# Performance work log

Measured on AMD Instinct MI355X. Metric: run time of the kernel, lower is better.

## Reference

```python
import jax, jax.numpy as jnp
import numpy as np


def setup_inputs() -> dict:
    key = jax.random.key(0)
    k = jax.random.split(key, 5)
    bs, n_heads, ch, n_obj, emb = 4, 8, 64, 8, 64
    ih = iw = 32
    T = ih * iw
    return {
        "qkv": jax.random.normal(k[0], (bs, 3 * n_heads * ch, T), dtype=jnp.float32),
        "bboxes": jax.random.uniform(k[1], (bs, n_obj, 5), dtype=jnp.float32),
        "null_prompt_emb": jax.random.normal(k[2], (bs, emb, T), dtype=jnp.float32),
        "prompt_emb": jax.random.normal(k[3], (bs, emb, T), dtype=jnp.float32),
        "W_prompt": jax.random.normal(k[4], (3 * n_heads * ch, emb), dtype=jnp.float32) * 0.02,
        "n_heads": n_heads,
        "image_h": ih,
        "image_w": iw,
    }


def _region_masks(bboxes, h, w):
    # Faithful translation of get_region: bbox unpacked as (x, y, width, height, obj_idx).
    # Returns float masks [b, n_obj, h*w].
    x, y, bw, bh = bboxes[..., 0], bboxes[..., 1], bboxes[..., 2], bboxes[..., 3]
    i0 = jnp.minimum(float(h) - 1.0, jnp.floor(y * h))
    j0 = jnp.minimum(float(w) - 1.0, jnp.floor(x * w))
    i1 = i0 + jnp.maximum(1.0, jnp.ceil(bh * h))
    j1 = j0 + jnp.maximum(1.0, jnp.ceil(bw * w))
    ii = jnp.arange(h, dtype=jnp.float32)
    jj = jnp.arange(w, dtype=jnp.float32)
    mi = (ii >= i0[..., None]) & (ii < i1[..., None])          # [b, n, h]
    mj = (jj >= j0[..., None]) & (jj < j1[..., None])          # [b, n, w]
    m = (mi[..., :, None] & mj[..., None, :]).astype(jnp.float32)  # [b, n, h, w]
    return m.reshape(m.shape[0], m.shape[1], h * w)


def reference(qkv, bboxes, null_prompt_emb, prompt_emb, W_prompt, n_heads, image_h, image_w):
    bs, width, T = qkv.shape
    ch = width // (3 * n_heads)
    scale = float(ch) ** -0.25  # 1/sqrt(sqrt(ch))

    def split3(x):
        x = x.reshape(bs * n_heads, 3 * ch, T)
        return x[:, :ch], x[:, ch:2 * ch], x[:, 2 * ch:]

    q, k, v = split3(qkv)
    # to_prompt_token is a 1x1 Conv1d (no bias) == matmul over the channel dim
    nq, nk, nv = split3(jnp.einsum('oc,bct->bot', W_prompt, null_prompt_emb))
    pq, pk, pv = split3(jnp.einsum('oc,bct->bot', W_prompt, prompt_emb))

    def attn(qh, kh, vh, col_mask=None):
        w = jnp.einsum('bct,bcs->bts', qh * scale, kh * scale)
        if col_mask is not None:
            w = jnp.where(col_mask[:, None, :] > 0.5, w, -1e9)
        w = jax.nn.softmax(w.astype(jnp.float32), axis=-1).astype(qh.dtype)
        return jnp.einsum('bts,bcs->btc', w, vh)  # [bs*heads, T, ch]

    # global (null-prompt) attention
    a_null = attn(q + nq, k + nk, v + nv)

    # per-object masked attention, blended by region masks
    masks = _region_masks(bboxes, image_h, image_w)       # [bs, n_obj, T]
    masks = jnp.repeat(masks, n_heads, axis=0)            # [(bs*heads), n_obj, T]
    qf, kf, vf = q + pq, k + pk, v + pv
    a_fg = jnp.zeros_like(a_null)
    counter = jnp.zeros((bs * n_heads, T, 1), dtype=jnp.float32)
    for o in range(masks.shape[1]):  # small fixed loop over objects
        m = masks[:, o]                                   # [bs*heads, T]
        a_fg = a_fg + m[:, :, None] * attn(qf, kf, vf, col_mask=m)
        counter = counter + m[:, :, None]
    fg = counter > 0.5
    a_final = jnp.where(fg, a_fg, a_null) / jnp.where(fg, counter, 1.0)
    return jnp.transpose(a_final, (0, 2, 1)).reshape(bs, n_heads * ch, T)
```

## Files before the change

### kernel.cpp

```cpp
#include <hip/hip_runtime.h>
#include <math.h>

#define BS 4
#define NH 8
#define TT 1024
#define WROWS 1536
#define NOBJ 8
#define NT 65536

#define QNT_OFF  0
#define KNT_OFF  2097152
#define VNCS_OFF 4194304
#define QFT_OFF  6291456
#define KFT_OFF  8388608
#define VFT_OFF  10485760

typedef __attribute__((ext_vector_type(8))) short short8;
typedef __attribute__((ext_vector_type(4))) float v4f;

__device__ __forceinline__ short f2bf(float f) {
    unsigned u = __float_as_uint(f);
    u = (u + 0x7FFF + ((u >> 16) & 1)) >> 16;
    return (short)u;
}
__device__ __forceinline__ unsigned p2(float a, float b) {
    return (unsigned)(unsigned short)f2bf(a) | ((unsigned)(unsigned short)f2bf(b) << 16);
}

__device__ __forceinline__ void get_region(const float* __restrict__ bb,
                                           int& i0, int& j0, int& hh, int& ww) {
    float x = bb[0], y = bb[1], bw = bb[2], bh = bb[3];
    float i0f = fminf(31.0f, floorf(y * 32.0f));
    float j0f = fminf(31.0f, floorf(x * 32.0f));
    float i1f = i0f + fmaxf(1.0f, ceilf(bh * 32.0f));
    float j1f = j0f + fmaxf(1.0f, ceilf(bw * 32.0f));
    i0 = (int)i0f; j0 = (int)j0f;
    int i1 = min(32, (int)i1f);
    int j1 = min(32, (int)j1f);
    hh = i1 - i0; ww = j1 - j0;
}

__global__ __launch_bounds__(256)
void fuse_kernel(const float* __restrict__ qkv, const float* __restrict__ nEmb,
                 const float* __restrict__ pEmb, const float* __restrict__ W,
                 short* __restrict__ wsS) {
    __shared__ float WtT[64][68];
    __shared__ float En[64][64];
    __shared__ float Ep[64][64];
    short* sbuf = (short*)&WtT[0][0];
    int t0 = blockIdx.x * 64;
    int r0 = blockIdx.y * 64;
    int b  = blockIdx.z;
    int tid = threadIdx.x;
    int half = tid >> 4;
    int q4 = (tid & 15) * 4;
#pragma unroll
    for (int p = 0; p < 4; ++p) {
        int rr = p * 16 + half;
        float4 w4 = *(const float4*)&W[(r0 + rr) * 64 + q4];
        WtT[q4 + 0][rr] = w4.x; WtT[q4 + 1][rr] = w4.y;
        WtT[q4 + 2][rr] = w4.z; WtT[q4 + 3][rr] = w4.w;
        int e = p * 16 + half;
        *(float4*)&En[e][q4] = *(const float4*)&nEmb[(b * 64 + e) * TT + t0 + q4];
        *(float4*)&Ep[e][q4] = *(const float4*)&pEmb[(b * 64 + e) * TT + t0 + q4];
    }
    __syncthreads();
    int tr = tid >> 4, tc = tid & 15;
    float an[4][4] = {{0.f}}, ap[4][4] = {{0.f}};
#pragma unroll 8
    for (int e = 0; e < 64; ++e) {
        float4 w4 = *(const float4*)&WtT[e][tr * 4];
        float4 n4 = *(const float4*)&En[e][tc * 4];
        float4 p4 = *(const float4*)&Ep[e][tc * 4];
        float w[4]  = {w4.x, w4.y, w4.z, w4.w};
        float nn[4] = {n4.x, n4.y, n4.z, n4.w};
        float pp[4] = {p4.x, p4.y, p4.z, p4.w};
#pragma unroll
        for (int i = 0; i < 4; ++i)
#pragma unroll
            for (int j = 0; j < 4; ++j) {
                an[i][j] += w[i] * nn[j];
                ap[i][j] += w[i] * pp[j];
            }
    }
    int sec = (r0 % 192) / 64;
    int h = r0 / 192, bh = b * 8 + h;
    float sc = (sec == 0) ? 0.125f : 1.0f;
#pragma unroll
    for (int i = 0; i < 4; ++i) {
        int r = r0 + tr * 4 + i;
        float4 x4 = *(const float4*)&qkv[(b * WROWS + r) * TT + t0 + tc * 4];
        an[i][0] = (an[i][0] + x4.x) * sc; an[i][1] = (an[i][1] + x4.y) * sc;
        an[i][2] = (an[i][2] + x4.z) * sc; an[i][3] = (an[i][3] + x4.w) * sc;
        ap[i][0] = (ap[i][0] + x4.x) * sc; ap[i][1] = (ap[i][1] + x4.y) * sc;
        ap[i][2] = (ap[i][2] + x4.z) * sc; ap[i][3] = (ap[i][3] + x4.w) * sc;
    }
    if (sec == 2) {
        short* Vn = wsS + VNCS_OFF + bh * NT;
#pragma unroll
        for (int i = 0; i < 4; ++i) {
            int c = tr * 4 + i;
            uint2 pk; pk.x = p2(an[i][0], an[i][1]); pk.y = p2(an[i][2], an[i][3]);
            *(uint2*)&Vn[c * TT + t0 + tc * 4] = pk;
        }
        short* dst = wsS + VFT_OFF + bh * NT + t0 * 64;
        __syncthreads();
#pragma unroll
        for (int i = 0; i < 4; ++i)
#pragma unroll
            for (int j = 0; j < 4; ++j)
                sbuf[(tc * 4 + j) * 72 + tr * 4 + i] = f2bf(ap[i][j]);
        __syncthreads();
#pragma unroll
        for (int rep = 0; rep < 2; ++rep) {
            int idx = rep * 256 + tid; int tl = idx >> 3, c8 = idx & 7;
            *(short8*)&dst[tl * 64 + c8 * 8] = *(const short8*)&sbuf[tl * 72 + c8 * 8];
        }
    } else {
        short* dn = wsS + (sec == 0 ? QNT_OFF : KNT_OFF) + bh * NT + t0 * 64;
        short* df = wsS + (sec == 0 ? QFT_OFF : KFT_OFF) + bh * NT + t0 * 64;
        __syncthreads();
#pragma unroll
        for (int i = 0; i < 4; ++i)
#pragma unroll
            for (int j = 0; j < 4; ++j)
                sbuf[(tc * 4 + j) * 72 + tr * 4 + i] = f2bf(an[i][j]);
        __syncthreads();
#pragma unroll
        for (int rep = 0; rep < 2; ++rep) {
            int idx = rep * 256 + tid; int tl = idx >> 3, c8 = idx & 7;
            *(short8*)&dn[tl * 64 + c8 * 8] = *(const short8*)&sbuf[tl * 72 + c8 * 8];
        }
        __syncthreads();
#pragma unroll
        for (int i = 0; i < 4; ++i)
#pragma unroll
            for (int j = 0; j < 4; ++j)
                sbuf[(tc * 4 + j) * 72 + tr * 4 + i] = f2bf(ap[i][j]);
        __syncthreads();
#pragma unroll
        for (int rep = 0; rep < 2; ++rep) {
            int idx = rep * 256 + tid; int tl = idx >> 3, c8 = idx & 7;
            *(short8*)&df[tl * 64 + c8 * 8] = *(const short8*)&sbuf[tl * 72 + c8 * 8];
        }
    }
}

__global__ __launch_bounds__(256)
void attn_fused(const short* __restrict__ wsS, const float* __restrict__ bboxes,
                float* __restrict__ out) {
    __shared__ __align__(16) short lds[13824];
    __shared__ unsigned short tmap[1024];
    short* Qs = lds;
    short* Ks = lds + 4608;
    short* Vs = lds + 9216;
    int rt = blockIdx.x, bh = blockIdx.y;
    int b = bh >> 3, h = bh & 7;
    int t0 = rt * 64;
    int tid = threadIdx.x;
    int w = tid >> 6, lane = tid & 63, ln = lane & 15, qd = lane >> 4;
    const short* QnT = wsS + QNT_OFF + bh * NT;
    const short* KnT = wsS + KNT_OFF + bh * NT;
    const short* Vn  = wsS + VNCS_OFF + bh * NT;
    const short* QfT = wsS + QFT_OFF + bh * NT;
    const short* KfT = wsS + KFT_OFF + bh * NT;
    const short* VfT = wsS + VFT_OFF + bh * NT;
    int sidx = tid, scell = sidx >> 3, sc8 = sidx & 7;
    int sidx2 = 256 + tid, scell2 = sidx2 >> 3, sc82 = sidx2 & 7;

    *(short8*)&Qs[scell * 72 + sc8 * 8]  = *(const short8*)&QnT[(t0 + scell) * 64 + sc8 * 8];
    *(short8*)&Qs[scell2 * 72 + sc82 * 8] = *(const short8*)&QnT[(t0 + scell2) * 64 + sc82 * 8];
    __syncthreads();
    short8 aq0 = *(const short8*)&Qs[(16 * w + ln) * 72 + qd * 8];
    short8 aq1 = *(const short8*)&Qs[(16 * w + ln) * 72 + 32 + qd * 8];
    v4f O[4]; float l[4];
#pragma unroll
    for (int r = 0; r < 4; ++r) l[r] = 0.f;
#pragma unroll
    for (int cc = 0; cc < 4; ++cc) O[cc] = (v4f){0.f, 0.f, 0.f, 0.f};
    short8 kreg[2], vreg[2];
    kreg[0] = *(const short8*)&KnT[scell * 64 + sc8 * 8];
    kreg[1] = *(const short8*)&KnT[scell2 * 64 + sc82 * 8];
    vreg[0] = *(const short8*)&Vn[scell * TT + sc8 * 8];
    vreg[1] = *(const short8*)&Vn[scell2 * TT + sc82 * 8];
    for (int ct = 0; ct < 16; ++ct) {
        __syncthreads();
        *(short8*)&Ks[scell * 72 + sc8 * 8]  = kreg[0];
        *(short8*)&Ks[scell2 * 72 + sc82 * 8] = kreg[1];
        *(short8*)&Vs[scell * 72 + sc8 * 8]  = vreg[0];
        *(short8*)&Vs[scell2 * 72 + sc82 * 8] = vreg[1];
        __syncthreads();
        if (ct < 15) {
            int s0 = (ct + 1) * 64;
            kreg[0] = *(const short8*)&KnT[(s0 + scell) * 64 + sc8 * 8];
            kreg[1] = *(const short8*)&KnT[(s0 + scell2) * 64 + sc82 * 8];
            vreg[0] = *(const short8*)&Vn[scell * TT + s0 + sc8 * 8];
            vreg[1] = *(const short8*)&Vn[scell2 * TT + s0 + sc82 * 8];
        }
        v4f S[4];
#pragma unroll
        for (int nn = 0; nn < 4; ++nn) {
            short8 b0 = *(const short8*)&Ks[(nn * 16 + ln) * 72 + qd * 8];
            short8 b1 = *(const short8*)&Ks[(nn * 16 + ln) * 72 + 32 + qd * 8];
            v4f z = (v4f){0.f, 0.f, 0.f, 0.f};
            z = __builtin_amdgcn_mfma_f32_16x16x32_bf16(aq0, b0, z, 0, 0, 0);
            z = __builtin_amdgcn_mfma_f32_16x16x32_bf16(aq1, b1, z, 0, 0, 0);
            S[nn] = z;
        }
#pragma unroll
        for (int r = 0; r < 4; ++r) {
            float e0 = __expf(S[0][r]);
            float e1 = __expf(S[1][r]);
            float e2 = __expf(S[2][r]);
            float e3 = __expf(S[3][r]);
            l[r] += e0 + e1 + e2 + e3;
            int prow = (w * 16 + 4 * qd + r) * 72;
            Qs[prow +  0 + ln] = f2bf(e0);
            Qs[prow + 16 + ln] = f2bf(e1);
            Qs[prow + 32 + ln] = f2bf(e2);
            Qs[prow + 48 + ln] = f2bf(e3);
        }
        short8 ap0 = *(const short8*)&Qs[(w * 16 + ln) * 72 + qd * 8];
        short8 ap1 = *(const short8*)&Qs[(w * 16 + ln) * 72 + 32 + qd * 8];
#pragma unroll
        for (int cc = 0; cc < 4; ++cc) {
            short8 bv0 = *(const short8*)&Vs[(cc * 16 + ln) * 72 + qd * 8];
            short8 bv1 = *(const short8*)&Vs[(cc * 16 + ln) * 72 + 32 + qd * 8];
            O[cc] = __builtin_amdgcn_mfma_f32_16x16x32_bf16(ap0, bv0, O[cc], 0, 0, 0);
            O[cc] = __builtin_amdgcn_mfma_f32_16x16x32_bf16(ap1, bv1, O[cc], 0, 0, 0);
        }
    }
    v4f Onull[4];
#pragma unroll
    for (int r = 0; r < 4; ++r) {
        float rs = l[r];
        rs += __shfl_xor(rs, 1, 64);
        rs += __shfl_xor(rs, 2, 64);
        rs += __shfl_xor(rs, 4, 64);
        rs += __shfl_xor(rs, 8, 64);
        float inv = 1.0f / rs;
#pragma unroll
        for (int cc = 0; cc < 4; ++cc) Onull[cc][r] = O[cc][r] * inv;
    }

    __syncthreads();
    *(short8*)&Qs[scell * 72 + sc8 * 8]  = *(const short8*)&QfT[(t0 + scell) * 64 + sc8 * 8];
    *(short8*)&Qs[scell2 * 72 + sc82 * 8] = *(const short8*)&QfT[(t0 + scell2) * 64 + sc82 * 8];
    __syncthreads();
    aq0 = *(const short8*)&Qs[(16 * w + ln) * 72 + qd * 8];
    aq1 = *(const short8*)&Qs[(16 * w + ln) * 72 + 32 + qd * 8];
    v4f Oacc[4]; float cnt[4];
#pragma unroll
    for (int r = 0; r < 4; ++r) cnt[r] = 0.f;
#pragma unroll
    for (int cc = 0; cc < 4; ++cc) Oacc[cc] = (v4f){0.f, 0.f, 0.f, 0.f};

    for (int o = 0; o < NOBJ; ++o) {
        int i0, j0, hh, ww;
        get_region(&bboxes[(b * NOBJ + o) * 5], i0, j0, hh, ww);
        int i1 = i0 + hh;
        if (i0 > 2 * rt + 1 || i1 <= 2 * rt) continue;
        int R = hh * ww;
        for (int idx = tid; idx < R; idx += 256) {
            int ri = idx / ww; int rj = idx - ri * ww;
            tmap[idx] = (unsigned short)((i0 + ri) * 32 + j0 + rj);
        }
        __syncthreads();
#pragma unroll
        for (int r = 0; r < 4; ++r) l[r] = 0.f;
#pragma unroll
        for (int cc = 0; cc < 4; ++cc) O[cc] = (v4f){0.f, 0.f, 0.f, 0.f};
        int nct = (R + 63) >> 6;
        {
            int tA = tmap[min(scell, R - 1)];
            int tB = tmap[min(scell2, R - 1)];
            kreg[0] = *(const short8*)&KfT[tA * 64 + sc8 * 8];
            kreg[1] = *(const short8*)&KfT[tB * 64 + sc82 * 8];
            vreg[0] = *(const short8*)&VfT[tA * 64 + sc8 * 8];
            vreg[1] = *(const short8*)&VfT[tB * 64 + sc82 * 8];
        }
        for (int ct = 0; ct < nct; ++ct) {
            int sb = ct * 64;
            __syncthreads();
            *(short8*)&Ks[scell * 72 + sc8 * 8]  = kreg[0];
            *(short8*)&Ks[scell2 * 72 + sc82 * 8] = kreg[1];
#pragma unroll
            for (int jj = 0; jj < 8; ++jj) {
                int j = (jj + sc8) & 7;
                Vs[(sc8 * 8 + j) * 72 + scell] = vreg[0][j];
            }
#pragma unroll
            for (int jj = 0; jj < 8; ++jj) {
                int j = (jj + sc82) & 7;
                Vs[(sc82 * 8 + j) * 72 + scell2] = vreg[1][j];
            }
            __syncthreads();
            if (ct + 1 < nct) {
                int s0 = sb + 64;
                int tA = tmap[min(s0 + scell, R - 1)];
                int tB = tmap[min(s0 + scell2, R - 1)];
                kreg[0] = *(const short8*)&KfT[tA * 64 + sc8 * 8];
                kreg[1] = *(const short8*)&KfT[tB * 64 + sc82 * 8];
                vreg[0] = *(const short8*)&VfT[tA * 64 + sc8 * 8];
                vreg[1] = *(const short8*)&VfT[tB * 64 + sc82 * 8];
            }
            v4f S[4];
#pragma unroll
            for (int nn = 0; nn < 4; ++nn) {
                short8 b0 = *(const short8*)&Ks[(nn * 16 + ln) * 72 + qd * 8];
                short8 b1 = *(const short8*)&Ks[(nn * 16 + ln) * 72 + 32 + qd * 8];
                v4f z = (v4f){0.f, 0.f, 0.f, 0.f};
                z = __builtin_amdgcn_mfma_f32_16x16x32_bf16(aq0, b0, z, 0, 0, 0);
                z = __builtin_amdgcn_mfma_f32_16x16x32_bf16(aq1, b1, z, 0, 0, 0);
                S[nn] = z;
            }
            float v0 = (sb +  0 + ln) < R ? 1.f : 0.f;
            float v1 = (sb + 16 + ln) < R ? 1.f : 0.f;
            float v2 = (sb + 32 + ln) < R ? 1.f : 0.f;
            float v3 = (sb + 48 + ln) < R ? 1.f : 0.f;
#pragma unroll
            for (int r = 0; r < 4; ++r) {
                float e0 = __expf(S[0][r]) * v0;
                float e1 = __expf(S[1][r]) * v1;
                float e2 = __expf(S[2][r]) * v2;
                float e3 = __expf(S[3][r]) * v3;
                l[r] += e0 + e1 + e2 + e3;
                int prow = (w * 16 + 4 * qd + r) * 72;
                Qs[prow +  0 + ln] = f2bf(e0);
                Qs[prow + 16 + ln] = f2bf(e1);
                Qs[prow + 32 + ln] = f2bf(e2);
                Qs[prow + 48 + ln] = f2bf(e3);
            }
            short8 ap0 = *(const short8*)&Qs[(w * 16 + ln) * 72 + qd * 8];
            short8 ap1 = *(const short8*)&Qs[(w * 16 + ln) * 72 + 32 + qd * 8];
#pragma unroll
            for (int cc = 0; cc < 4; ++cc) {
                short8 bv0 = *(const short8*)&Vs[(cc * 16 + ln) * 72 + qd * 8];
                short8 bv1 = *(const short8*)&Vs[(cc * 16 + ln) * 72 + 32 + qd * 8];
                O[cc] = __builtin_amdgcn_mfma_f32_16x16x32_bf16(ap0, bv0, O[cc], 0, 0, 0);
                O[cc] = __builtin_amdgcn_mfma_f32_16x16x32_bf16(ap1, bv1, O[cc], 0, 0, 0);
            }
        }
#pragma unroll
        for (int r = 0; r < 4; ++r) {
            float rs = l[r];
            rs += __shfl_xor(rs, 1, 64);
            rs += __shfl_xor(rs, 2, 64);
            rs += __shfl_xor(rs, 4, 64);
            rs += __shfl_xor(rs, 8, 64);
            float inv = 1.0f / rs;
            int t = t0 + 16 * w + 4 * qd + r;
            int ti = t >> 5, tj = t & 31;
            bool in = (ti >= i0) && (ti < i1) && (tj >= j0) && (tj < j0 + ww);
            if (in) {
                cnt[r] += 1.f;
#pragma unroll
                for (int cc = 0; cc < 4; ++cc) Oacc[cc][r] += O[cc][r] * inv;
            }
        }
    }

    __syncthreads();
    float* Ot = (float*)lds;
#pragma unroll
    for (int r = 0; r < 4; ++r) {
        int tl = 16 * w + 4 * qd + r;
        float icnt = cnt[r] > 0.f ? 1.0f / cnt[r] : 0.f;
#pragma unroll
        for (int cc = 0; cc < 4; ++cc) {
            float val = cnt[r] > 0.f ? Oacc[cc][r] * icnt : Onull[cc][r];
            Ot[(cc * 16 + ln) * 68 + tl] = val;
        }
    }
    __syncthreads();
    int obase = (b * 512 + h * 64) * TT + t0;
#pragma unroll
    for (int rep = 0; rep < 4; ++rep) {
        int idx = rep * 256 + tid; int c = idx >> 4, t4 = (idx & 15) * 4;
        *(float4*)&out[obase + c * TT + t4] = *(float4*)&Ot[c * 68 + t4];
    }
}

extern "C" void kernel_launch(void* const* d_in, const int* in_sizes, int n_in,
                              void* d_out, int out_size, void* d_ws, size_t ws_size,
                              hipStream_t stream) {
    const float* qkv    = (const float*)d_in[0];
    const float* bboxes = (const float*)d_in[1];
    const float* nEmb   = (const float*)d_in[2];
    const float* pEmb   = (const float*)d_in[3];
    const float* W      = (const float*)d_in[4];
    short* wsS = (short*)d_ws;
    float* out = (float*)d_out;

    fuse_kernel<<<dim3(16, 24, 4), 256, 0, stream>>>(qkv, nEmb, pEmb, W, wsS);
    attn_fused<<<dim3(16, 32), 256, 0, stream>>>(wsS, bboxes, out);
}
```

Measured before the change: 160.5 us.

## Tile attention per image row and skip null attention for fully covered rows

Each block now handles one 32-token image row with 128 threads instead of 64 tokens with 256 threads, which doubles the grid. Per-row object intersection and column-coverage bitmasks are computed up front. The global null-prompt attention is skipped when the object boxes cover the whole row, and per-object work is limited to intersecting objects. P is packed to bf16 by truncation with wider LDS stores, and the K row order is permuted so the P write pattern matches. This adds more complex indexing, truncation instead of rounding in the bf16 conversion, and less parallelism per block.

```diff
diff --git a/kernel.cpp b/kernel.cpp
--- a/kernel.cpp
+++ b/kernel.cpp
@@ -25,6 +25,9 @@
 }
 __device__ __forceinline__ unsigned p2(float a, float b) {
     return (unsigned)(unsigned short)f2bf(a) | ((unsigned)(unsigned short)f2bf(b) << 16);
+}
+__device__ __forceinline__ unsigned p2t(float a, float b) {
+    return (__float_as_uint(a) >> 16) | (__float_as_uint(b) & 0xFFFF0000u);
 }
 
 __device__ __forceinline__ void get_region(const float* __restrict__ bb,
@@ -146,17 +149,17 @@
     }
 }
 
-__global__ __launch_bounds__(256)
+__global__ __launch_bounds__(128)
 void attn_fused(const short* __restrict__ wsS, const float* __restrict__ bboxes,
                 float* __restrict__ out) {
-    __shared__ __align__(16) short lds[13824];
+    __shared__ __align__(16) short lds[11520];
     __shared__ unsigned short tmap[1024];
     short* Qs = lds;
-    short* Ks = lds + 4608;
-    short* Vs = lds + 9216;
-    int rt = blockIdx.x, bh = blockIdx.y;
+    short* Ks = lds + 2304;
+    short* Vs = lds + 6912;
+    int bh = blockIdx.x, rt = blockIdx.y;
     int b = bh >> 3, h = bh & 7;
-    int t0 = rt * 64;
+    int t0 = rt * 32;
     int tid = threadIdx.x;
     int w = tid >> 6, lane = tid & 63, ln = lane & 15, qd = lane >> 4;
     const short* QnT = wsS + QNT_OFF + bh * NT;
@@ -165,144 +168,63 @@
     const short* QfT = wsS + QFT_OFF + bh * NT;
     const short* KfT = wsS + KFT_OFF + bh * NT;
     const short* VfT = wsS + VFT_OFF + bh * NT;
-    int sidx = tid, scell = sidx >> 3, sc8 = sidx & 7;
-    int sidx2 = 256 + tid, scell2 = sidx2 >> 3, sc82 = sidx2 & 7;
-
-    *(short8*)&Qs[scell * 72 + sc8 * 8]  = *(const short8*)&QnT[(t0 + scell) * 64 + sc8 * 8];
-    *(short8*)&Qs[scell2 * 72 + sc82 * 8] = *(const short8*)&QnT[(t0 + scell2) * 64 + sc82 * 8];
-    __syncthreads();
-    short8 aq0 = *(const short8*)&Qs[(16 * w + ln) * 72 + qd * 8];
-    short8 aq1 = *(const short8*)&Qs[(16 * w + ln) * 72 + 32 + qd * 8];
-    v4f O[4]; float l[4];
-#pragma unroll
-    for (int r = 0; r < 4; ++r) l[r] = 0.f;
-#pragma unroll
-    for (int cc = 0; cc < 4; ++cc) O[cc] = (v4f){0.f, 0.f, 0.f, 0.f};
-    short8 kreg[2], vreg[2];
-    kreg[0] = *(const short8*)&KnT[scell * 64 + sc8 * 8];
-    kreg[1] = *(const short8*)&KnT[scell2 * 64 + sc82 * 8];
-    vreg[0] = *(const short8*)&Vn[scell * TT + sc8 * 8];
-    vreg[1] = *(const short8*)&Vn[scell2 * TT + sc82 * 8];
-    for (int ct = 0; ct < 16; ++ct) {
-        __syncthreads();
-        *(short8*)&Ks[scell * 72 + sc8 * 8]  = kreg[0];
-        *(short8*)&Ks[scell2 * 72 + sc82 * 8] = kreg[1];
-        *(short8*)&Vs[scell * 72 + sc8 * 8]  = vreg[0];
-        *(short8*)&Vs[scell2 * 72 + sc82 * 8] = vreg[1];
-        __syncthreads();
-        if (ct < 15) {
-            int s0 = (ct + 1) * 64;
-            kreg[0] = *(const short8*)&KnT[(s0 + scell) * 64 + sc8 * 8];
-            kreg[1] = *(const short8*)&KnT[(s0 + scell2) * 64 + sc82 * 8];
-            vreg[0] = *(const short8*)&Vn[scell * TT + s0 + sc8 * 8];
-            vreg[1] = *(const short8*)&Vn[scell2 * TT + s0 + sc82 * 8];
-        }
-        v4f S[4];
-#pragma unroll
-        for (int nn = 0; nn < 4; ++nn) {
-            short8 b0 = *(const short8*)&Ks[(nn * 16 + ln) * 72 + qd * 8];
-            short8 b1 = *(const short8*)&Ks[(nn * 16 + ln) * 72 + 32 + qd * 8];
-            v4f z = (v4f){0.f, 0.f, 0.f, 0.f};
-            z = __builtin_amdgcn_mfma_f32_16x16x32_bf16(aq0, b0, z, 0, 0, 0);
-            z = __builtin_amdgcn_mfma_f32_16x16x32_bf16(aq1, b1, z, 0, 0, 0);
-            S[nn] = z;
-        }
-#pragma unroll
-        for (int r = 0; r < 4; ++r) {
-            float e0 = __expf(S[0][r]);
-            float e1 = __expf(S[1][r]);
-            float e2 = __expf(S[2][r]);
-            float e3 = __expf(S[3][r]);
-            l[r] += e0 + e1 + e2 + e3;
-            int prow = (w * 16 + 4 * qd + r) * 72;
-            Qs[prow +  0 + ln] = f2bf(e0);
-            Qs[prow + 16 + ln] = f2bf(e1);
-            Qs[prow + 32 + ln] = f2bf(e2);
-            Qs[prow + 48 + ln] = f2bf(e3);
-        }
-        short8 ap0 = *(const short8*)&Qs[(w * 16 + ln) * 72 + qd * 8];
-        short8 ap1 = *(const short8*)&Qs[(w * 16 + ln) * 72 + 32 + qd * 8];
-#pragma unroll
-        for (int cc = 0; cc < 4; ++cc) {
-            short8 bv0 = *(const short8*)&Vs[(cc * 16 + ln) * 72 + qd * 8];
-            short8 bv1 = *(const short8*)&Vs[(cc * 16 + ln) * 72 + 32 + qd * 8];
-            O[cc] = __builtin_amdgcn_mfma_f32_16x16x32_bf16(ap0, bv0, O[cc], 0, 0, 0);
-            O[cc] = __builtin_amdgcn_mfma_f32_16x16x32_bf16(ap1, bv1, O[cc], 0, 0, 0);
-        }
-    }
-    v4f Onull[4];
-#pragma unroll
-    for (int r = 0; r < 4; ++r) {
-        float rs = l[r];
-        rs += __shfl_xor(rs, 1, 64);
-        rs += __shfl_xor(rs, 2, 64);
-        rs += __shfl_xor(rs, 4, 64);
-        rs += __shfl_xor(rs, 8, 64);
-        float inv = 1.0f / rs;
-#pragma unroll
-        for (int cc = 0; cc < 4; ++cc) Onull[cc][r] = O[cc][r] * inv;
-    }
-
-    __syncthreads();
-    *(short8*)&Qs[scell * 72 + sc8 * 8]  = *(const short8*)&QfT[(t0 + scell) * 64 + sc8 * 8];
-    *(short8*)&Qs[scell2 * 72 + sc82 * 8] = *(const short8*)&QfT[(t0 + scell2) * 64 + sc82 * 8];
-    __syncthreads();
-    aq0 = *(const short8*)&Qs[(16 * w + ln) * 72 + qd * 8];
-    aq1 = *(const short8*)&Qs[(16 * w + ln) * 72 + 32 + qd * 8];
-    v4f Oacc[4]; float cnt[4];
-#pragma unroll
-    for (int r = 0; r < 4; ++r) cnt[r] = 0.f;
-#pragma unroll
-    for (int cc = 0; cc < 4; ++cc) Oacc[cc] = (v4f){0.f, 0.f, 0.f, 0.f};
-
+
+    unsigned inter = 0u, cover = 0u;
     for (int o = 0; o < NOBJ; ++o) {
         int i0, j0, hh, ww;
         get_region(&bboxes[(b * NOBJ + o) * 5], i0, j0, hh, ww);
-        int i1 = i0 + hh;
-        if (i0 > 2 * rt + 1 || i1 <= 2 * rt) continue;
-        int R = hh * ww;
-        for (int idx = tid; idx < R; idx += 256) {
-            int ri = idx / ww; int rj = idx - ri * ww;
-            tmap[idx] = (unsigned short)((i0 + ri) * 32 + j0 + rj);
-        }
-        __syncthreads();
+        if (i0 <= rt && rt < i0 + hh) {
+            inter |= (1u << o);
+            unsigned wm = (ww >= 32) ? 0xFFFFFFFFu : (((1u << ww) - 1u) << j0);
+            cover |= wm;
+        }
+    }
+
+    v4f Onull[4];
+#pragma unroll
+    for (int cc = 0; cc < 4; ++cc) Onull[cc] = (v4f){0.f, 0.f, 0.f, 0.f};
+
+    if (cover != 0xFFFFFFFFu) {
+#pragma unroll
+        for (int rep = 0; rep < 2; ++rep) {
+            int idx = rep * 128 + tid; int cell = idx >> 3, o8 = idx & 7;
+            *(short8*)&Qs[cell * 72 + o8 * 8] =
+                *(const short8*)&QnT[(t0 + cell) * 64 + o8 * 8];
+        }
+        __syncthreads();
+        short8 aq0 = *(const short8*)&Qs[(16 * w + ln) * 72 + qd * 8];
+        short8 aq1 = *(const short8*)&Qs[(16 * w + ln) * 72 + 32 + qd * 8];
+        v4f O[4]; float l[4];
 #pragma unroll
         for (int r = 0; r < 4; ++r) l[r] = 0.f;
 #pragma unroll
         for (int cc = 0; cc < 4; ++cc) O[cc] = (v4f){0.f, 0.f, 0.f, 0.f};
-        int nct = (R + 63) >> 6;
-        {
-            int tA = tmap[min(scell, R - 1)];
-            int tB = tmap[min(scell2, R - 1)];
-            kreg[0] = *(const short8*)&KfT[tA * 64 + sc8 * 8];
-            kreg[1] = *(const short8*)&KfT[tB * 64 + sc82 * 8];
-            vreg[0] = *(const short8*)&VfT[tA * 64 + sc8 * 8];
-            vreg[1] = *(const short8*)&VfT[tB * 64 + sc82 * 8];
-        }
-        for (int ct = 0; ct < nct; ++ct) {
-            int sb = ct * 64;
+        short8 kreg[4], vreg[4];
+#pragma unroll
+        for (int rep = 0; rep < 4; ++rep) {
+            int idx = rep * 128 + tid; int cell = idx >> 3, o8 = idx & 7;
+            int pc = 4 * (cell & 15) + (cell >> 4);
+            kreg[rep] = *(const short8*)&KnT[pc * 64 + o8 * 8];
+            vreg[rep] = *(const short8*)&Vn[cell * TT + o8 * 8];
+        }
+        for (int ct = 0; ct < 16; ++ct) {
             __syncthreads();
-            *(short8*)&Ks[scell * 72 + sc8 * 8]  = kreg[0];
-            *(short8*)&Ks[scell2 * 72 + sc82 * 8] = kreg[1];
-#pragma unroll
-            for (int jj = 0; jj < 8; ++jj) {
-                int j = (jj + sc8) & 7;
-                Vs[(sc8 * 8 + j) * 72 + scell] = vreg[0][j];
-            }
-#pragma unroll
-            for (int jj = 0; jj < 8; ++jj) {
-                int j = (jj + sc82) & 7;
-                Vs[(sc82 * 8 + j) * 72 + scell2] = vreg[1][j];
+#pragma unroll
+            for (int rep = 0; rep < 4; ++rep) {
+                int idx = rep * 128 + tid; int cell = idx >> 3, o8 = idx & 7;
+                *(short8*)&Ks[cell * 72 + o8 * 8] = kreg[rep];
+                *(short8*)&Vs[cell * 72 + o8 * 8] = vreg[rep];
             }
             __syncthreads();
-            if (ct + 1 < nct) {
-                int s0 = sb + 64;
-                int tA = tmap[min(s0 + scell, R - 1)];
-                int tB = tmap[min(s0 + scell2, R - 1)];
-                kreg[0] = *(const short8*)&KfT[tA * 64 + sc8 * 8];
-                kreg[1] = *(const short8*)&KfT[tB * 64 + sc82 * 8];
-                vreg[0] = *(const short8*)&VfT[tA * 64 + sc8 * 8];
-                vreg[1] = *(const short8*)&VfT[tB * 64 + sc82 * 8];
+            if (ct < 15) {
+                int s0 = (ct + 1) * 64;
+#pragma unroll
+                for (int rep = 0; rep < 4; ++rep) {
+                    int idx = rep * 128 + tid; int cell = idx >> 3, o8 = idx & 7;
+                    int pc = 4 * (cell & 15) + (cell >> 4);
+                    kreg[rep] = *(const short8*)&KnT[(s0 + pc) * 64 + o8 * 8];
+                    vreg[rep] = *(const short8*)&Vn[cell * TT + s0 + o8 * 8];
+                }
             }
             v4f S[4];
 #pragma unroll
@@ -314,22 +236,15 @@
                 z = __builtin_amdgcn_mfma_f32_16x16x32_bf16(aq1, b1, z, 0, 0, 0);
                 S[nn] = z;
             }
-            float v0 = (sb +  0 + ln) < R ? 1.f : 0.f;
-            float v1 = (sb + 16 + ln) < R ? 1.f : 0.f;
-            float v2 = (sb + 32 + ln) < R ? 1.f : 0.f;
-            float v3 = (sb + 48 + ln) < R ? 1.f : 0.f;
 #pragma unroll
             for (int r = 0; r < 4; ++r) {
-                float e0 = __expf(S[0][r]) * v0;
-                float e1 = __expf(S[1][r]) * v1;
-                float e2 = __expf(S[2][r]) * v2;
-                float e3 = __expf(S[3][r]) * v3;
+                float e0 = __expf(S[0][r]);
+                float e1 = __expf(S[1][r]);
+                float e2 = __expf(S[2][r]);
+                float e3 = __expf(S[3][r]);
                 l[r] += e0 + e1 + e2 + e3;
-                int prow = (w * 16 + 4 * qd + r) * 72;
-                Qs[prow +  0 + ln] = f2bf(e0);
-                Qs[prow + 16 + ln] = f2bf(e1);
-                Qs[prow + 32 + ln] = f2bf(e2);
-                Qs[prow + 48 + ln] = f2bf(e3);
+                uint2 pk; pk.x = p2t(e0, e1); pk.y = p2t(e2, e3);
+                *(uint2*)&Qs[(w * 16 + 4 * qd + r) * 72 + 4 * ln] = pk;
             }
             short8 ap0 = *(const short8*)&Qs[(w * 16 + ln) * 72 + qd * 8];
             short8 ap1 = *(const short8*)&Qs[(w * 16 + ln) * 72 + 32 + qd * 8];
@@ -349,19 +264,135 @@
             rs += __shfl_xor(rs, 4, 64);
             rs += __shfl_xor(rs, 8, 64);
             float inv = 1.0f / rs;
-            int t = t0 + 16 * w + 4 * qd + r;
-            int ti = t >> 5, tj = t & 31;
-            bool in = (ti >= i0) && (ti < i1) && (tj >= j0) && (tj < j0 + ww);
-            if (in) {
-                cnt[r] += 1.f;
-#pragma unroll
-                for (int cc = 0; cc < 4; ++cc) Oacc[cc][r] += O[cc][r] * inv;
+#pragma unroll
+            for (int cc = 0; cc < 4; ++cc) Onull[cc][r] = O[cc][r] * inv;
+        }
+    }
+
+    v4f Oacc[4]; float cnt[4];
+#pragma unroll
+    for (int r = 0; r < 4; ++r) cnt[r] = 0.f;
+#pragma unroll
+    for (int cc = 0; cc < 4; ++cc) Oacc[cc] = (v4f){0.f, 0.f, 0.f, 0.f};
+
+    if (inter != 0u) {
+        __syncthreads();
+#pragma unroll
+        for (int rep = 0; rep < 2; ++rep) {
+            int idx = rep * 128 + tid; int cell = idx >> 3, o8 = idx & 7;
+            *(short8*)&Qs[cell * 72 + o8 * 8] =
+                *(const short8*)&QfT[(t0 + cell) * 64 + o8 * 8];
+        }
+        __syncthreads();
+        short8 aq0 = *(const short8*)&Qs[(16 * w + ln) * 72 + qd * 8];
+        short8 aq1 = *(const short8*)&Qs[(16 * w + ln) * 72 + 32 + qd * 8];
+        for (int o = 0; o < NOBJ; ++o) {
+            if (!((inter >> o) & 1u)) continue;
+            int i0, j0, hh, ww;
+            get_region(&bboxes[(b * NOBJ + o) * 5], i0, j0, hh, ww);
+            int R = hh * ww;
+            for (int idx = tid; idx < R; idx += 128) {
+                int ri = idx / ww; int rj = idx - ri * ww;
+                tmap[idx] = (unsigned short)((i0 + ri) * 32 + j0 + rj);
+            }
+            __syncthreads();
+            v4f O[4]; float l[4];
+#pragma unroll
+            for (int r = 0; r < 4; ++r) l[r] = 0.f;
+#pragma unroll
+            for (int cc = 0; cc < 4; ++cc) O[cc] = (v4f){0.f, 0.f, 0.f, 0.f};
+            int nct = (R + 63) >> 6;
+            short8 kreg[4], vreg[4];
+#pragma unroll
+            for (int rep = 0; rep < 4; ++rep) {
+                int idx = rep * 128 + tid; int cell = idx >> 3, o8 = idx & 7;
+                int pc = 4 * (cell & 15) + (cell >> 4);
+                int tk = tmap[min(pc, R - 1)];
+                int tv = tmap[min(cell, R - 1)];
+                kreg[rep] = *(const short8*)&KfT[tk * 64 + o8 * 8];
+                vreg[rep] = *(const short8*)&VfT[tv * 64 + o8 * 8];
+            }
+            for (int ct = 0; ct < nct; ++ct) {
+                int sb = ct * 64;
+                __syncthreads();
+#pragma unroll
+                for (int rep = 0; rep < 4; ++rep) {
+                    int idx = rep * 128 + tid; int cell = idx >> 3, o8 = idx & 7;
+                    *(short8*)&Ks[cell * 72 + o8 * 8] = kreg[rep];
+#pragma unroll
+                    for (int jj = 0; jj < 8; ++jj) {
+                        int j = (jj + o8) & 7;
+                        Vs[(o8 * 8 + j) * 72 + cell] = vreg[rep][j];
+                    }
+                }
+                __syncthreads();
+                if (ct + 1 < nct) {
+                    int s0 = sb + 64;
+#pragma unroll
+                    for (int rep = 0; rep < 4; ++rep) {
+                        int idx = rep * 128 + tid; int cell = idx >> 3, o8 = idx & 7;
+                        int pc = 4 * (cell & 15) + (cell >> 4);
+                        int tk = tmap[min(s0 + pc, R - 1)];
+                        int tv = tmap[min(s0 + cell, R - 1)];
+                        kreg[rep] = *(const short8*)&KfT[tk * 64 + o8 * 8];
+                        vreg[rep] = *(const short8*)&VfT[tv * 64 + o8 * 8];
+                    }
+                }
+                v4f S[4];
+#pragma unroll
+                for (int nn = 0; nn < 4; ++nn) {
+                    short8 b0 = *(const short8*)&Ks[(nn * 16 + ln) * 72 + qd * 8];
+                    short8 b1 = *(const short8*)&Ks[(nn * 16 + ln) * 72 + 32 + qd * 8];
+                    v4f z = (v4f){0.f, 0.f, 0.f, 0.f};
+                    z = __builtin_amdgcn_mfma_f32_16x16x32_bf16(aq0, b0, z, 0, 0, 0);
+                    z = __builtin_amdgcn_mfma_f32_16x16x32_bf16(aq1, b1, z, 0, 0, 0);
+                    S[nn] = z;
+                }
+                float v0 = (sb + 4 * ln + 0) < R ? 1.f : 0.f;
+                float v1 = (sb + 4 * ln + 1) < R ? 1.f : 0.f;
+                float v2 = (sb + 4 * ln + 2) < R ? 1.f : 0.f;
+                float v3 = (sb + 4 * ln + 3) < R ? 1.f : 0.f;
+#pragma unroll
+                for (int r = 0; r < 4; ++r) {
+                    float e0 = __expf(S[0][r]) * v0;
+                    float e1 = __expf(S[1][r]) * v1;
+                    float e2 = __expf(S[2][r]) * v2;
+                    float e3 = __expf(S[3][r]) * v3;
+                    l[r] += e0 + e1 + e2 + e3;
+                    uint2 pk; pk.x = p2t(e0, e1); pk.y = p2t(e2, e3);
+                    *(uint2*)&Qs[(w * 16 + 4 * qd + r) * 72 + 4 * ln] = pk;
+                }
+                short8 ap0 = *(const short8*)&Qs[(w * 16 + ln) * 72 + qd * 8];
+                short8 ap1 = *(const short8*)&Qs[(w * 16 + ln) * 72 + 32 + qd * 8];
+#pragma unroll
+                for (int cc = 0; cc < 4; ++cc) {
+                    short8 bv0 = *(const short8*)&Vs[(cc * 16 + ln) * 72 + qd * 8];
+                    short8 bv1 = *(const short8*)&Vs[(cc * 16 + ln) * 72 + 32 + qd * 8];
+                    O[cc] = __builtin_amdgcn_mfma_f32_16x16x32_bf16(ap0, bv0, O[cc], 0, 0, 0);
+                    O[cc] = __builtin_amdgcn_mfma_f32_16x16x32_bf16(ap1, bv1, O[cc], 0, 0, 0);
+                }
+            }
+#pragma unroll
+            for (int r = 0; r < 4; ++r) {
+                float rs = l[r];
+                rs += __shfl_xor(rs, 1, 64);
+                rs += __shfl_xor(rs, 2, 64);
+                rs += __shfl_xor(rs, 4, 64);
+                rs += __shfl_xor(rs, 8, 64);
+                float inv = 1.0f / rs;
+                int tj = 16 * w + 4 * qd + r;
+                bool in = (tj >= j0) && (tj < j0 + ww);
+                if (in) {
+                    cnt[r] += 1.f;
+#pragma unroll
+                    for (int cc = 0; cc < 4; ++cc) Oacc[cc][r] += O[cc][r] * inv;
+                }
             }
         }
     }
 
     __syncthreads();
-    float* Ot = (float*)lds;
+    float* Ot = (float*)(lds + 2304);
 #pragma unroll
     for (int r = 0; r < 4; ++r) {
         int tl = 16 * w + 4 * qd + r;
@@ -369,15 +400,15 @@
 #pragma unroll
         for (int cc = 0; cc < 4; ++cc) {
             float val = cnt[r] > 0.f ? Oacc[cc][r] * icnt : Onull[cc][r];
-            Ot[(cc * 16 + ln) * 68 + tl] = val;
+            Ot[(cc * 16 + ln) * 36 + tl] = val;
         }
     }
     __syncthreads();
     int obase = (b * 512 + h * 64) * TT + t0;
 #pragma unroll
     for (int rep = 0; rep < 4; ++rep) {
-        int idx = rep * 256 + tid; int c = idx >> 4, t4 = (idx & 15) * 4;
-        *(float4*)&out[obase + c * TT + t4] = *(float4*)&Ot[c * 68 + t4];
+        int idx = rep * 128 + tid; int c = idx >> 3, t4 = (idx & 7) * 4;
+        *(float4*)&out[obase + c * TT + t4] = *(float4*)&Ot[c * 36 + t4];
     }
 }
 
@@ -393,5 +424,5 @@
     float* out = (float*)d_out;
 
     fuse_kernel<<<dim3(16, 24, 4), 256, 0, stream>>>(qkv, nEmb, pEmb, W, wsS);
-    attn_fused<<<dim3(16, 32), 256, 0, stream>>>(wsS, bboxes, out);
-}
+    attn_fused<<<dim3(32, 32), 128, 0, stream>>>(wsS, bboxes, out);
+}
```

New measurement: 170.1 us. 1.06x slower.
